# Kernel tuning notes

Measured on AMD Instinct MI355X. Metric: run time of the kernel, lower is better.

## Reference

```python
import jax, jax.numpy as jnp
import numpy as np

POOLING_RATIO = 0.5  # matches init kwarg
N_NODES = 16384
N_EDGES = 524288
D_FEAT = 128


def setup_inputs() -> dict:
    key = jax.random.key(0)
    k1, k2, k3, k4 = jax.random.split(key, 4)
    return {
        "pos": jax.random.normal(k1, (N_NODES, 3), jnp.float32),
        "feat": jax.random.normal(k2, (N_NODES, D_FEAT), jnp.float32),
        "src": jax.random.randint(k3, (N_EDGES,), 0, N_NODES, jnp.int32),
        "dst": jax.random.randint(k4, (N_EDGES,), 0, N_NODES, jnp.int32),
        "batch_size": 4,
    }


def _fps(p, k):
    # Farthest point sampling on one cloud p: [n, 3]. Deterministic start at idx 0
    # (DGL uses a random start; we fix it for reproducibility).
    n = p.shape[0]
    def step(carry, _):
        dists, last = carry  # dists: min sq-dist to selected set so far
        d = jnp.sum((p - p[last]) ** 2, axis=-1)
        dists = jnp.minimum(dists, d)
        nxt = jnp.argmax(dists).astype(jnp.int32)
        return (dists, nxt), last
    init = (jnp.full((n,), 1e10, p.dtype), jnp.asarray(0, jnp.int32))
    _, idx = jax.lax.scan(step, init, None, length=k)
    return idx  # [k]


def reference(pos, feat, src, dst, batch_size):
    N = pos.shape[0]
    n_points = N // batch_size
    k = round(n_points * (1.0 - POOLING_RATIO))  # downsampled points per cloud

    # ---- farthest point sampling per cloud ----
    p = pos.reshape(batch_size, n_points, pos.shape[-1])  # [B, n, 3]
    fp = jax.vmap(lambda q: _fps(q, k))(p)                # [B, k] local ids
    offs = (jnp.arange(batch_size, dtype=jnp.int32) * n_points)[:, None]
    fp_idx = (fp + offs).reshape(-1)                      # [B*k] global ids

    # ---- copy_u + mean aggregation on the FULL graph (G.update_all) ----
    deg = jax.ops.segment_sum(jnp.ones_like(dst, dtype=feat.dtype), dst, num_segments=N)
    agg = jax.ops.segment_sum(feat[src], dst, num_segments=N)  # [N, D]
    agg = agg / jnp.maximum(deg, 1.0)[:, None]  # nodes with no in-edges stay 0

    # ---- induced subgraph gather ----
    M = fp_idx.shape[0]
    sub_x = pos[fp_idx]      # [M, 3]
    sub_feat = agg[fp_idx]   # [M, D]

    # induced subgraph edges: keep original edges whose endpoints are both sampled
    inv = jnp.full((N,), -1, jnp.int32).at[fp_idx].set(jnp.arange(M, dtype=jnp.int32))
    ls, ld = inv[src], inv[dst]
    edge_mask = (ls >= 0) & (ld >= 0)
    ls = jnp.where(edge_mask, ls, 0)
    ld = jnp.where(edge_mask, ld, 0)

    # per-edge displacement and norm on subgraph positions
    d = jnp.where(edge_mask[:, None], sub_x[ld] - sub_x[ls], 0.0)  # [E, 3]
    w = jnp.sqrt(jnp.sum(d ** 2, axis=-1, keepdims=True))          # [E, 1]

    return sub_x, sub_feat, d, w, edge_mask, fp_idx
```

## Files before the change

### kernel.cpp

```cpp
#include <hip/hip_runtime.h>
#include <math.h>

#define N_NODES 16384
#define N_EDGES 524288
#define D_FEAT  128
#define BATCH   4
#define NPTS    4096
#define KSEL    2048
#define MSEL    (BATCH*KSEL)

#define X16(F) F(0) F(1) F(2) F(3) F(4) F(5) F(6) F(7) \
               F(8) F(9) F(10) F(11) F(12) F(13) F(14) F(15)


template <int CTRL>
__device__ __forceinline__ float dpp_f32(float v)
{
    return __int_as_float(
        __builtin_amdgcn_update_dpp(0, __float_as_int(v), CTRL, 0xf, 0xf, true));
}
template <int CTRL>
__device__ __forceinline__ unsigned dpp_u32(unsigned v)
{
    return (unsigned)__builtin_amdgcn_update_dpp(0, (int)v, CTRL, 0xf, 0xf, true);
}

__launch_bounds__(256, 1)
__global__ void fps_kernel(const float* __restrict__ pos,
                           int* __restrict__ fp_int,
                           int* __restrict__ inv,
                           float* __restrict__ out_subx,
                           float* __restrict__ out_fp)
{
    __shared__ float sx[NPTS];
    __shared__ float sy[NPTS];
    __shared__ float sz[NPTS];
    __shared__ int   sel[KSEL];
    __shared__ unsigned long long pwv[2][4];

    const int b    = blockIdx.x;
    const int tid  = threadIdx.x;
    const int lane = tid & 63;
    const int wv   = tid >> 6;

    const float* gp = pos + (size_t)b * NPTS * 3;
    for (int i = tid; i < NPTS; i += 256) {
        sx[i] = gp[3 * i + 0];
        sy[i] = gp[3 * i + 1];
        sz[i] = gp[3 * i + 2];
    }
    __syncthreads();

#define DECL(J) float x##J, y##J, z##J, d##J;
    X16(DECL)
#undef DECL
#define LOAD(J) { int li = (J)*256 + tid; x##J = sx[li]; y##J = sy[li]; z##J = sz[li]; d##J = 1e10f; }
    X16(LOAD)
#undef LOAD

    int cur = 0;
    for (int t = 0; t < KSEL; ++t) {
        if (tid == 0) sel[t] = cur;
        float qx = sx[cur];
        float qy = sy[cur];
        float qz = sz[cur];

#define UPD(J) { \
        float dx = __fsub_rn(x##J, qx); \
        float dy = __fsub_rn(y##J, qy); \
        float dz = __fsub_rn(z##J, qz); \
        float dd = __fadd_rn(__fadd_rn(__fmul_rn(dx, dx), __fmul_rn(dy, dy)), \
                             __fmul_rn(dz, dz)); \
        d##J = fminf(d##J, dd); }
        X16(UPD)
#undef UPD

#define NODE(VA, JA, VB, JB, VO, JO) \
        float VO = (VB > VA) ? VB : VA; int JO = (VB > VA) ? JB : JA;
        NODE(d0,  0, d1,  1,  v01, j01)  NODE(d2,  2, d3,  3,  v23, j23)
        NODE(d4,  4, d5,  5,  v45, j45)  NODE(d6,  6, d7,  7,  v67, j67)
        NODE(d8,  8, d9,  9,  v89, j89)  NODE(d10,10, d11,11,  vab, jab)
        NODE(d12,12, d13,13,  vcd, jcd)  NODE(d14,14, d15,15,  vef, jef)
        NODE(v01, j01, v23, j23, vA, jA) NODE(v45, j45, v67, j67, vB, jB)
        NODE(v89, j89, vab, jab, vC, jC) NODE(vcd, jcd, vef, jef, vD, jD)
        NODE(vA, jA, vB, jB, vE, jE)     NODE(vC, jC, vD, jD, vF, jF)
        NODE(vE, jE, vF, jF, bv, bj)
#undef NODE
        int bi = bj * 256 + tid;

        float rv = bv;
        rv = fmaxf(rv, dpp_f32<0x111>(rv));
        rv = fmaxf(rv, dpp_f32<0x112>(rv));
        rv = fmaxf(rv, dpp_f32<0x114>(rv));
        rv = fmaxf(rv, dpp_f32<0x118>(rv));
        rv = fmaxf(rv, dpp_f32<0x142>(rv));
        rv = fmaxf(rv, dpp_f32<0x143>(rv));
        unsigned smax_u = (unsigned)__builtin_amdgcn_readlane(__float_as_int(rv), 63);

        unsigned cand = (__float_as_uint(bv) == smax_u) ? ~(unsigned)bi : 0u;
        cand = max(cand, dpp_u32<0x111>(cand));
        cand = max(cand, dpp_u32<0x112>(cand));
        cand = max(cand, dpp_u32<0x114>(cand));
        cand = max(cand, dpp_u32<0x118>(cand));
        cand = max(cand, dpp_u32<0x142>(cand));
        cand = max(cand, dpp_u32<0x143>(cand));
        unsigned winv = (unsigned)__builtin_amdgcn_readlane((int)cand, 63);

        unsigned long long p = (((unsigned long long)smax_u) << 32) | winv;

        int par = t & 1;
        if (lane == 0) pwv[par][wv] = p;
        __syncthreads();

        unsigned long long c0 = pwv[par][0];
        unsigned long long c1 = pwv[par][1];
        unsigned long long c2 = pwv[par][2];
        unsigned long long c3 = pwv[par][3];
        unsigned long long m01 = (c0 > c1) ? c0 : c1;
        unsigned long long m23 = (c2 > c3) ? c2 : c3;
        unsigned long long mm  = (m01 > m23) ? m01 : m23;
        cur = (int)(~(unsigned)(mm & 0xffffffffULL));
    }
    __syncthreads();

    for (int t = tid; t < KSEL; t += 256) {
        int c = sel[t];
        int g = b * NPTS + c;
        int m = b * KSEL + t;
        fp_int[m] = g;
        inv[g] = m;
        out_fp[m] = (float)g;
        out_subx[m * 3 + 0] = sx[c];
        out_subx[m * 3 + 1] = sy[c];
        out_subx[m * 3 + 2] = sz[c];
    }
}

__global__ void deg_kernel(const int* __restrict__ dst, int* __restrict__ deg)
{
    int e = blockIdx.x * blockDim.x + threadIdx.x;
    if (e < N_EDGES) atomicAdd(&deg[dst[e]], 1);
}

__global__ void scan_kernel(const int* __restrict__ deg, int* __restrict__ row_ptr)
{
    __shared__ int part[1024];
    int tid = threadIdx.x;
    int base = tid * 16;
    int local[16];
    int s = 0;
#pragma unroll
    for (int j = 0; j < 16; ++j) { local[j] = s; s += deg[base + j]; }
    part[tid] = s;
    __syncthreads();
    for (int off = 1; off < 1024; off <<= 1) {
        int v = part[tid];
        int add = (tid >= off) ? part[tid - off] : 0;
        __syncthreads();
        part[tid] = v + add;
        __syncthreads();
    }
    int prefix = (tid == 0) ? 0 : part[tid - 1];
#pragma unroll
    for (int j = 0; j < 16; ++j) row_ptr[base + j] = prefix + local[j];
    if (tid == 1023) row_ptr[N_NODES] = part[1023];
}

__global__ void scatter_kernel(const int* __restrict__ src, const int* __restrict__ dst,
                               const int* __restrict__ row_ptr, int* __restrict__ cursor,
                               int* __restrict__ col)
{
    int e = blockIdx.x * blockDim.x + threadIdx.x;
    if (e < N_EDGES) {
        int d0 = dst[e];
        int r = atomicAdd(&cursor[d0], 1);
        col[row_ptr[d0] + r] = src[e];
    }
}

__global__ void agg_edge_kernel(const float* __restrict__ feat,
                                const int* __restrict__ fp_int,
                                const int* __restrict__ row_ptr,
                                const int* __restrict__ col,
                                const int* __restrict__ deg,
                                float* __restrict__ out_subfeat,
                                const int* __restrict__ src,
                                const int* __restrict__ dst,
                                const int* __restrict__ inv,
                                const float* __restrict__ subx,
                                float* __restrict__ outd,
                                float* __restrict__ outw,
                                float* __restrict__ outm)
{
    if (blockIdx.x < 2048) {
        int wid  = (blockIdx.x * blockDim.x + threadIdx.x) >> 6;
        int lane = threadIdx.x & 63;
        int v  = fp_int[wid];
        int s0 = row_ptr[v];
        int s1 = row_ptr[v + 1];
        float a0 = 0.0f, a1 = 0.0f;
        for (int e = s0; e < s1; ++e) {
            int s = col[e];
            const float2* f2 = (const float2*)(feat + (size_t)s * D_FEAT);
            float2 vv = f2[lane];
            a0 += vv.x;
            a1 += vv.y;
        }
        float dv = fmaxf((float)deg[v], 1.0f);
        float* o = out_subfeat + (size_t)wid * D_FEAT + lane * 2;
        o[0] = a0 / dv;
        o[1] = a1 / dv;
    } else {
        int e = (blockIdx.x - 2048) * blockDim.x + threadIdx.x;
        int ls = inv[src[e]];
        int ld = inv[dst[e]];
        bool mk = (ls >= 0) && (ld >= 0);
        float dx = 0.0f, dy = 0.0f, dz = 0.0f;
        if (mk) {
            dx = __fsub_rn(subx[ld * 3 + 0], subx[ls * 3 + 0]);
            dy = __fsub_rn(subx[ld * 3 + 1], subx[ls * 3 + 1]);
            dz = __fsub_rn(subx[ld * 3 + 2], subx[ls * 3 + 2]);
        }
        float w = sqrtf(__fadd_rn(__fadd_rn(__fmul_rn(dx, dx), __fmul_rn(dy, dy)),
                                  __fmul_rn(dz, dz)));
        outd[e * 3 + 0] = dx;
        outd[e * 3 + 1] = dy;
        outd[e * 3 + 2] = dz;
        outw[e] = w;
        outm[e] = mk ? 1.0f : 0.0f;
    }
}

extern "C" void kernel_launch(void* const* d_in, const int* in_sizes, int n_in,
                              void* d_out, int out_size, void* d_ws, size_t ws_size,
                              hipStream_t stream)
{
    const float* pos  = (const float*)d_in[0];
    const float* feat = (const float*)d_in[1];
    const int*   src  = (const int*)d_in[2];
    const int*   dst  = (const int*)d_in[3];

    float* out = (float*)d_out;
    float* out_subx    = out;
    float* out_subfeat = out_subx + (size_t)MSEL * 3;
    float* out_d       = out_subfeat + (size_t)MSEL * D_FEAT;
    float* out_w       = out_d + (size_t)N_EDGES * 3;
    float* out_m       = out_w + (size_t)N_EDGES;
    float* out_fp      = out_m + (size_t)N_EDGES;

    int* fp_int  = (int*)d_ws;
    int* inv     = fp_int + MSEL;
    int* deg     = inv + N_NODES;
    int* row_ptr = deg + N_NODES;
    int* cursor  = row_ptr + (N_NODES+1);
    int* col     = cursor + N_NODES;

    (void)hipMemsetAsync(inv,    0xFF, (size_t)N_NODES * 4, stream);
    (void)hipMemsetAsync(deg,    0,    (size_t)N_NODES * 4, stream);
    (void)hipMemsetAsync(cursor, 0,    (size_t)N_NODES * 4, stream);

    deg_kernel<<<N_EDGES / 256, 256, 0, stream>>>(dst, deg);
    scan_kernel<<<1, 1024, 0, stream>>>(deg, row_ptr);
    scatter_kernel<<<N_EDGES / 256, 256, 0, stream>>>(src, dst, row_ptr, cursor, col);

    fps_kernel<<<BATCH, 256, 0, stream>>>(pos, fp_int, inv, out_subx, out_fp);

    agg_edge_kernel<<<4096, 256, 0, stream>>>(feat, fp_int, row_ptr, col, deg,
                                              out_subfeat, src, dst, inv, out_subx,
                                              out_d, out_w, out_m);
}
```

Measured before the change: 1.419 ms.

## Fuse degree counting into FPS launch and pack FPS distance math

After: 1.339 ms. -5.6%, faster.

```diff
diff --git a/kernel.cpp b/kernel.cpp
--- a/kernel.cpp
+++ b/kernel.cpp
@@ -9,28 +9,36 @@
 #define KSEL    2048
 #define MSEL    (BATCH*KSEL)
 
-#define X16(F) F(0) F(1) F(2) F(3) F(4) F(5) F(6) F(7) \
-               F(8) F(9) F(10) F(11) F(12) F(13) F(14) F(15)
-
+typedef float f32x2 __attribute__((ext_vector_type(2)));
+
+#define PK_ADD(D,A,B) asm("v_pk_add_f32 %0, %1, %2" : "=v"(D) : "v"(A), "v"(B))
+#define PK_MUL(D,A,B) asm("v_pk_mul_f32 %0, %1, %2" : "=v"(D) : "v"(A), "v"(B))
+
+#define X8(F) F(0) F(1) F(2) F(3) F(4) F(5) F(6) F(7)
 
 template <int CTRL>
-__device__ __forceinline__ float dpp_f32(float v)
-{
-    return __int_as_float(
-        __builtin_amdgcn_update_dpp(0, __float_as_int(v), CTRL, 0xf, 0xf, true));
-}
-template <int CTRL>
-__device__ __forceinline__ unsigned dpp_u32(unsigned v)
-{
-    return (unsigned)__builtin_amdgcn_update_dpp(0, (int)v, CTRL, 0xf, 0xf, true);
+__device__ __forceinline__ unsigned long long dpp_u64(unsigned long long p)
+{
+    unsigned slo = (unsigned)__builtin_amdgcn_update_dpp(
+        0, (int)(unsigned)p, CTRL, 0xf, 0xf, true);
+    unsigned shi = (unsigned)__builtin_amdgcn_update_dpp(
+        0, (int)(unsigned)(p >> 32), CTRL, 0xf, 0xf, true);
+    return (((unsigned long long)shi) << 32) | slo;
+}
+__device__ __forceinline__ unsigned long long max_u64(unsigned long long a,
+                                                      unsigned long long b)
+{
+    return (b > a) ? b : a;
 }
 
 __launch_bounds__(256, 1)
-__global__ void fps_kernel(const float* __restrict__ pos,
-                           int* __restrict__ fp_int,
-                           int* __restrict__ inv,
-                           float* __restrict__ out_subx,
-                           float* __restrict__ out_fp)
+__global__ void fps_deg_kernel(const float* __restrict__ pos,
+                               int* __restrict__ fp_int,
+                               int* __restrict__ inv,
+                               float* __restrict__ out_subx,
+                               float* __restrict__ out_fp,
+                               const int* __restrict__ dst,
+                               int* __restrict__ deg)
 {
     __shared__ float sx[NPTS];
     __shared__ float sy[NPTS];
@@ -38,6 +46,12 @@
     __shared__ int   sel[KSEL];
     __shared__ unsigned long long pwv[2][4];
 
+    if (blockIdx.x >= BATCH) {
+        int e = (blockIdx.x - BATCH) * 256 + threadIdx.x;
+        atomicAdd(&deg[dst[e]], 1);
+        return;
+    }
+
     const int b    = blockIdx.x;
     const int tid  = threadIdx.x;
     const int lane = tid & 63;
@@ -51,75 +65,70 @@
     }
     __syncthreads();
 
-#define DECL(J) float x##J, y##J, z##J, d##J;
-    X16(DECL)
+#define DECL(M) f32x2 x##M, y##M, z##M, d##M;
+    X8(DECL)
 #undef DECL
-#define LOAD(J) { int li = (J)*256 + tid; x##J = sx[li]; y##J = sy[li]; z##J = sz[li]; d##J = 1e10f; }
-    X16(LOAD)
+#define LOAD(M) { \
+        int l0 = (2*(M))*256 + tid, l1 = (2*(M)+1)*256 + tid; \
+        x##M.x = sx[l0]; x##M.y = sx[l1]; \
+        y##M.x = sy[l0]; y##M.y = sy[l1]; \
+        z##M.x = sz[l0]; z##M.y = sz[l1]; \
+        d##M.x = 1e10f;  d##M.y = 1e10f; }
+    X8(LOAD)
 #undef LOAD
 
+    float qx = sx[0], qy = sy[0], qz = sz[0];
     int cur = 0;
+
     for (int t = 0; t < KSEL; ++t) {
         if (tid == 0) sel[t] = cur;
-        float qx = sx[cur];
-        float qy = sy[cur];
-        float qz = sz[cur];
-
-#define UPD(J) { \
-        float dx = __fsub_rn(x##J, qx); \
-        float dy = __fsub_rn(y##J, qy); \
-        float dz = __fsub_rn(z##J, qz); \
-        float dd = __fadd_rn(__fadd_rn(__fmul_rn(dx, dx), __fmul_rn(dy, dy)), \
-                             __fmul_rn(dz, dz)); \
-        d##J = fminf(d##J, dd); }
-        X16(UPD)
-#undef UPD
-
-#define NODE(VA, JA, VB, JB, VO, JO) \
-        float VO = (VB > VA) ? VB : VA; int JO = (VB > VA) ? JB : JA;
-        NODE(d0,  0, d1,  1,  v01, j01)  NODE(d2,  2, d3,  3,  v23, j23)
-        NODE(d4,  4, d5,  5,  v45, j45)  NODE(d6,  6, d7,  7,  v67, j67)
-        NODE(d8,  8, d9,  9,  v89, j89)  NODE(d10,10, d11,11,  vab, jab)
-        NODE(d12,12, d13,13,  vcd, jcd)  NODE(d14,14, d15,15,  vef, jef)
-        NODE(v01, j01, v23, j23, vA, jA) NODE(v45, j45, v67, j67, vB, jB)
-        NODE(v89, j89, vab, jab, vC, jC) NODE(vcd, jcd, vef, jef, vD, jD)
-        NODE(vA, jA, vB, jB, vE, jE)     NODE(vC, jC, vD, jD, vF, jF)
-        NODE(vE, jE, vF, jF, bv, bj)
-#undef NODE
-        int bi = bj * 256 + tid;
-
-        float rv = bv;
-        rv = fmaxf(rv, dpp_f32<0x111>(rv));
-        rv = fmaxf(rv, dpp_f32<0x112>(rv));
-        rv = fmaxf(rv, dpp_f32<0x114>(rv));
-        rv = fmaxf(rv, dpp_f32<0x118>(rv));
-        rv = fmaxf(rv, dpp_f32<0x142>(rv));
-        rv = fmaxf(rv, dpp_f32<0x143>(rv));
-        unsigned smax_u = (unsigned)__builtin_amdgcn_readlane(__float_as_int(rv), 63);
-
-        unsigned cand = (__float_as_uint(bv) == smax_u) ? ~(unsigned)bi : 0u;
-        cand = max(cand, dpp_u32<0x111>(cand));
-        cand = max(cand, dpp_u32<0x112>(cand));
-        cand = max(cand, dpp_u32<0x114>(cand));
-        cand = max(cand, dpp_u32<0x118>(cand));
-        cand = max(cand, dpp_u32<0x142>(cand));
-        cand = max(cand, dpp_u32<0x143>(cand));
-        unsigned winv = (unsigned)__builtin_amdgcn_readlane((int)cand, 63);
-
-        unsigned long long p = (((unsigned long long)smax_u) << 32) | winv;
+
+        f32x2 nqx, nqy, nqz;
+        nqx.x = -qx; nqx.y = -qx;
+        nqy.x = -qy; nqy.y = -qy;
+        nqz.x = -qz; nqz.y = -qz;
+
+        float bv = -1.0f;
+        int   bj = 0;
+#define UPD2(M) { \
+        f32x2 dx, dy, dz, mx, my, mz, s1, dd; \
+        PK_ADD(dx, x##M, nqx); PK_ADD(dy, y##M, nqy); PK_ADD(dz, z##M, nqz); \
+        PK_MUL(mx, dx, dx); PK_MUL(my, dy, dy); PK_MUL(mz, dz, dz); \
+        PK_ADD(s1, mx, my); PK_ADD(dd, s1, mz); \
+        float n0 = fminf(d##M.x, dd.x); d##M.x = n0; \
+        if (n0 > bv) { bv = n0; bj = 2*(M); } \
+        float n1 = fminf(d##M.y, dd.y); d##M.y = n1; \
+        if (n1 > bv) { bv = n1; bj = 2*(M)+1; } }
+        X8(UPD2)
+#undef UPD2
+
+        int bi = (bj << 8) + tid;
+
+        unsigned long long p =
+            (((unsigned long long)__float_as_uint(bv)) << 32) |
+            (unsigned)(~bi);
+
+        p = max_u64(p, dpp_u64<0x111>(p));
+        p = max_u64(p, dpp_u64<0x112>(p));
+        p = max_u64(p, dpp_u64<0x114>(p));
+        p = max_u64(p, dpp_u64<0x118>(p));
+        p = max_u64(p, dpp_u64<0x142>(p));
+        p = max_u64(p, dpp_u64<0x143>(p));
 
         int par = t & 1;
-        if (lane == 0) pwv[par][wv] = p;
+        if (lane == 63) pwv[par][wv] = p;
         __syncthreads();
 
         unsigned long long c0 = pwv[par][0];
         unsigned long long c1 = pwv[par][1];
         unsigned long long c2 = pwv[par][2];
         unsigned long long c3 = pwv[par][3];
-        unsigned long long m01 = (c0 > c1) ? c0 : c1;
-        unsigned long long m23 = (c2 > c3) ? c2 : c3;
-        unsigned long long mm  = (m01 > m23) ? m01 : m23;
+        unsigned long long m01 = (c1 > c0) ? c1 : c0;
+        unsigned long long m23 = (c3 > c2) ? c3 : c2;
+        unsigned long long mm  = (m23 > m01) ? m23 : m01;
         cur = (int)(~(unsigned)(mm & 0xffffffffULL));
+
+        qx = sx[cur]; qy = sy[cur]; qz = sz[cur];
     }
     __syncthreads();
 
@@ -134,12 +143,6 @@
         out_subx[m * 3 + 1] = sy[c];
         out_subx[m * 3 + 2] = sz[c];
     }
-}
-
-__global__ void deg_kernel(const int* __restrict__ dst, int* __restrict__ deg)
-{
-    int e = blockIdx.x * blockDim.x + threadIdx.x;
-    if (e < N_EDGES) atomicAdd(&deg[dst[e]], 1);
 }
 
 __global__ void scan_kernel(const int* __restrict__ deg, int* __restrict__ row_ptr)
@@ -259,11 +262,11 @@
     (void)hipMemsetAsync(deg,    0,    (size_t)N_NODES * 4, stream);
     (void)hipMemsetAsync(cursor, 0,    (size_t)N_NODES * 4, stream);
 
-    deg_kernel<<<N_EDGES / 256, 256, 0, stream>>>(dst, deg);
+    fps_deg_kernel<<<BATCH + N_EDGES / 256, 256, 0, stream>>>(
+        pos, fp_int, inv, out_subx, out_fp, dst, deg);
+
     scan_kernel<<<1, 1024, 0, stream>>>(deg, row_ptr);
     scatter_kernel<<<N_EDGES / 256, 256, 0, stream>>>(src, dst, row_ptr, cursor, col);
-
-    fps_kernel<<<BATCH, 256, 0, stream>>>(pos, fp_int, inv, out_subx, out_fp);
 
     agg_edge_kernel<<<4096, 256, 0, stream>>>(feat, fp_int, row_ptr, col, deg,
                                               out_subfeat, src, dst, inv, out_subx,
```
